# Kernel optimization log

Hardware: AMD Instinct MI355X
Metric: run time of the kernel (lower is better)

## Reference

```python
import jax, jax.numpy as jnp
import numpy as np

N_CHAINS, L, N, D, K, H, FF = 8192, 128, 100000, 256, 8, 4, 1024
LN_EPS = 1e-5  # torch LayerNorm default
EPS = 1e-8     # module eps for mean-pool denom


def _ln(x, g, b):
    mu = jnp.mean(x, axis=-1, keepdims=True)
    var = jnp.mean((x - mu) ** 2, axis=-1, keepdims=True)
    return (x - mu) * jax.lax.rsqrt(var + LN_EPS) * g + b


def setup_inputs() -> dict:
    key = jax.random.key(0)
    ks = jax.random.split(key, 24)
    s = 1.0 / np.sqrt(D)
    inp = {
        "v": jax.random.normal(ks[0], (N, D), jnp.float32),
        "batch_idx": jax.random.randint(ks[1], (N_CHAINS, L), 0, N),
        "mask": jax.random.uniform(ks[2], (N_CHAINS, L)) > 0.5,
        "count": jax.random.randint(ks[3], (N_CHAINS,), 0, 128).astype(jnp.float32),
        "rank_scores": jax.random.normal(ks[4], (N_CHAINS, L), jnp.float32),
        "pos_embed": jnp.zeros((1, K, D), jnp.float32),
        "w_qkv": jax.random.normal(ks[5], (3 * D, D), jnp.float32) * s,
        "b_qkv": jnp.zeros((3 * D,), jnp.float32),
        "w_o": jax.random.normal(ks[6], (D, D), jnp.float32) * s,
        "b_o": jnp.zeros((D,), jnp.float32),
        "ln1_g": jnp.ones((D,), jnp.float32),
        "ln1_b": jnp.zeros((D,), jnp.float32),
        "ln2_g": jnp.ones((D,), jnp.float32),
        "ln2_b": jnp.zeros((D,), jnp.float32),
        "w_ff1": jax.random.normal(ks[7], (FF, D), jnp.float32) * s,
        "b_ff1": jnp.zeros((FF,), jnp.float32),
        "w_ff2": jax.random.normal(ks[8], (D, FF), jnp.float32) / np.sqrt(FF),
        "b_ff2": jnp.zeros((D,), jnp.float32),
        "w_out1": jax.random.normal(ks[9], (FF, D + 1), jnp.float32) * s,
        "b_out1": jnp.zeros((FF,), jnp.float32),
        "w_out2": jax.random.normal(ks[10], (D, FF), jnp.float32) / np.sqrt(FF),
        "b_out2": jnp.zeros((D,), jnp.float32),
    }
    return inp


def reference(v, batch_idx, mask, count, rank_scores, pos_embed, w_qkv, b_qkv,
              w_o, b_o, ln1_g, ln1_b, ln2_g, ln2_b, w_ff1, b_ff1, w_ff2, b_ff2,
              w_out1, b_out1, w_out2, b_out2):
    neg = jnp.finfo(jnp.float32).min
    # --- top-k relevance selection among masked positions ---
    masked_scores = jnp.where(mask, rank_scores.astype(jnp.float32), neg)
    _, top_idx = jax.lax.top_k(masked_scores, K)                # [n, K]
    picked = jnp.take_along_axis(mask, top_idx, axis=1)
    sortable = jnp.where(picked, top_idx, L)                     # sentinel L
    sortable = jnp.sort(sortable, axis=1)
    picked = sortable < L
    safe_idx = jnp.where(picked, sortable, 0)                    # [n, K]
    # gather-pack: v[batch_idx][safe_idx] == v[batch_idx gathered at safe_idx]
    member_idx = jnp.take_along_axis(batch_idx, safe_idx, axis=1)
    packed = v[member_idx] * picked[..., None].astype(v.dtype)   # [n, K, D]

    x = packed + pos_embed[:, :K, :]
    kpm = ~picked                                                # True = pad
    empty = jnp.all(kpm, axis=1)
    kpm = kpm.at[:, 0].set(jnp.where(empty, False, kpm[:, 0]))

    # --- one pre-LN transformer encoder layer (gelu, dropout=0) ---
    dh = D // H
    h = _ln(x, ln1_g, ln1_b)
    qkv = h @ w_qkv.T + b_qkv                                    # [n, K, 3D]
    q, k, val = jnp.split(qkv, 3, axis=-1)
    q = q.reshape(-1, K, H, dh)
    k = k.reshape(-1, K, H, dh)
    val = val.reshape(-1, K, H, dh)
    scores = jnp.einsum('bqhd,bkhd->bhqk', q, k) / np.sqrt(dh)
    scores = jnp.where(kpm[:, None, None, :], neg, scores)
    attn = jax.nn.softmax(scores, axis=-1)
    o = jnp.einsum('bhqk,bkhd->bqhd', attn, val).reshape(-1, K, D)
    x = x + (o @ w_o.T + b_o)
    h = _ln(x, ln2_g, ln2_b)
    x = x + jax.nn.gelu(h @ w_ff1.T + b_ff1, approximate=False) @ w_ff2.T + b_ff2

    # --- masked mean pool + log-count feature + MLP head ---
    pf = picked.astype(x.dtype)
    denom = jnp.clip(jnp.sum(pf, axis=1, keepdims=True), EPS, None)
    pooled = jnp.sum(x * pf[..., None], axis=1) / denom
    pooled = jnp.where(jnp.any(picked, axis=1, keepdims=True), pooled, 0.0)
    feat = jnp.concatenate([pooled, jnp.log1p(count.astype(x.dtype))[:, None]], axis=-1)
    return jax.nn.gelu(feat @ w_out1.T + b_out1, approximate=False) @ w_out2.T + b_out2
```

## Files before the change

kernel.cpp:

```cpp
#include <hip/hip_runtime.h>


#define DIM   256
#define LSEQ  128
#define KTOK  8

typedef __bf16 bf16x8 __attribute__((ext_vector_type(8)));
typedef float  f32x4  __attribute__((ext_vector_type(4)));
typedef unsigned short u16x8 __attribute__((ext_vector_type(8)));

__device__ __forceinline__ f32x4 mfma16(bf16x8 a, bf16x8 b, f32x4 c) {
  return __builtin_amdgcn_mfma_f32_16x16x32_bf16(a, b, c, 0, 0, 0);
}

__device__ __forceinline__ unsigned short f2bf(float f) {
  unsigned u = __float_as_uint(f);
  u = (u + 0x7FFFu + ((u >> 16) & 1u)) >> 16;
  return (unsigned short)u;
}

__device__ __forceinline__ float gelu_fast(float x) {
  const float y = 0.7978845608f * __builtin_fmaf(0.044715f * x * x, x, x);
  const float e = __expf(2.f * y);
  const float t = 1.f - 2.f * __builtin_amdgcn_rcpf(e + 1.f);
  return 0.5f * x * (1.f + t);
}

struct Stage32 { u16x8 r[4]; };
__device__ __forceinline__ void stage_load(Stage32& st, const unsigned short* __restrict__ g, int tid) {
  #pragma unroll
  for (int i = 0; i < 4; ++i) st.r[i] = *(const u16x8*)&g[(tid + i * 512) * 8];
}
__device__ __forceinline__ void stage_commit(const Stage32& st, unsigned short* l, int tid) {
  #pragma unroll
  for (int i = 0; i < 4; ++i) *(u16x8*)&l[(tid + i * 512) * 8] = st.r[i];
}

__device__ __forceinline__ void pack_region(
    const float* __restrict__ src, unsigned short* __restrict__ dst,
    int g, int KC, int Ksrc, int Klim)
{
  const int ln = g & 63;
  const int t = g >> 6;
  const int s = t % KC;
  const int ntile = t / KC;
  const int row = ntile * 16 + (ln & 15);
  const int c0 = s * 32 + (ln >> 4) * 8;
  u16x8 o;
  #pragma unroll
  for (int j = 0; j < 8; ++j) {
    float val = (c0 + j < Klim) ? src[(long)row * Ksrc + c0 + j] : 0.f;
    o[j] = f2bf(val);
  }
  *(u16x8*)&dst[(long)g * 8] = o;
}

__device__ __forceinline__ void pack_region_kmaj(
    const float* __restrict__ src, unsigned short* __restrict__ dst,
    int g, int NT, int Ksrc)
{
  const int ln = g & 63;
  const int t = g >> 6;
  const int ntile = t % NT;
  const int s = t / NT;
  const int row = ntile * 16 + (ln & 15);
  const int c0 = s * 32 + (ln >> 4) * 8;
  u16x8 o;
  #pragma unroll
  for (int j = 0; j < 8; ++j) o[j] = f2bf(src[(long)row * Ksrc + c0 + j]);
  *(u16x8*)&dst[(long)g * 8] = o;
}

#define PREP_GROUPS 172032
__global__ __launch_bounds__(256) void k_prep(
    const float* __restrict__ wqkv, const float* __restrict__ wo,
    const float* __restrict__ wff1, const float* __restrict__ wff2,
    const float* __restrict__ wout1, const float* __restrict__ wout2,
    unsigned short* __restrict__ oq, unsigned short* __restrict__ oo,
    unsigned short* __restrict__ of1, unsigned short* __restrict__ of2,
    unsigned short* __restrict__ oo1, unsigned short* __restrict__ oo2)
{
  int g = blockIdx.x * 256 + threadIdx.x;
  if (g < 24576) { pack_region(wqkv, oq, g, 8, 256, 256); return; }
  g -= 24576;
  if (g < 8192)  { pack_region(wo, oo, g, 8, 256, 256); return; }
  g -= 8192;
  if (g < 32768) { pack_region(wff1, of1, g, 8, 256, 256); return; }
  g -= 32768;
  if (g < 32768) { pack_region_kmaj(wff2, of2, g, 16, 1024); return; }
  g -= 32768;
  if (g < 40960) { pack_region(wout1, oo1, g, 10, 257, 257); return; }
  g -= 40960;
  if (g < 32768) { pack_region_kmaj(wout2, oo2, g, 16, 1024); }
}

__global__ __launch_bounds__(256) void k_sel(
    const float* __restrict__ v, const int* __restrict__ batch_idx,
    const int* __restrict__ mask, const float* __restrict__ rank_scores,
    const float* __restrict__ pos_embed,
    const float* __restrict__ ln1g, const float* __restrict__ ln1b,
    float* __restrict__ X, unsigned short* __restrict__ H1p,
    int* __restrict__ NPICK)
{
  const int c = blockIdx.x;
  const int tid = threadIdx.x;
  __shared__ int s_mem[KTOK];
  __shared__ int s_np;

  if (tid < 64) {
    const int l = tid;
    unsigned long long key[2];
    #pragma unroll
    for (int t = 0; t < 2; ++t) {
      int p = l + 64 * t;
      int mk = mask[c * LSEQ + p];
      float s = rank_scores[c * LSEQ + p];
      unsigned u = __float_as_uint(s);
      u = (u & 0x80000000u) ? ~u : (u | 0x80000000u);
      unsigned long long kk =
          ((unsigned long long)u << 32) | (unsigned long long)(0xFFFFFFFFu - (unsigned)p);
      key[t] = mk ? kk : 0ull;
    }
    int w[KTOK];
    #pragma unroll
    for (int r = 0; r < KTOK; ++r) w[r] = 0x7FFFFFFF;
    int np = 0;
    for (int r = 0; r < KTOK; ++r) {
      unsigned long long best = key[0] > key[1] ? key[0] : key[1];
      for (int off = 32; off > 0; off >>= 1) {
        unsigned long long o = __shfl_xor(best, off, 64);
        if (o > best) best = o;
      }
      if (best == 0ull) break;
      int idx = (int)(0xFFFFFFFFu - (unsigned)(best & 0xFFFFFFFFull));
      w[np++] = idx;
      if (key[0] == best) key[0] = 0ull;
      if (key[1] == best) key[1] = 0ull;
    }
    #pragma unroll
    for (int a = 0; a < KTOK - 1; ++a)
      #pragma unroll
      for (int b2 = 0; b2 < KTOK - 1 - a; ++b2) {
        int x0 = w[b2], x1 = w[b2 + 1];
        w[b2] = min(x0, x1); w[b2 + 1] = max(x0, x1);
      }
    if (l < KTOK) s_mem[l] = (l < np) ? batch_idx[c * LSEQ + w[l]] : -1;
    if (l == 0) { s_np = np; NPICK[c] = np; }
  }
  __syncthreads();

  const int np = s_np;
  const int j = tid >> 5, q = tid & 31;
  const int r = s_mem[j];
  const float4* v4  = (const float4*)v;
  const float4* pe4 = (const float4*)pos_embed;
  float4* X4 = (float4*)X;

  float4 xv[2];
  #pragma unroll
  for (int rep = 0; rep < 2; ++rep) {
    const int f = 2 * q + rep;
    float4 pe = pe4[j * 64 + f];
    float4 val = make_float4(0.f, 0.f, 0.f, 0.f);
    if (j < np) val = v4[(long)r * 64 + f];
    xv[rep].x = val.x + pe.x; xv[rep].y = val.y + pe.y;
    xv[rep].z = val.z + pe.z; xv[rep].w = val.w + pe.w;
    X4[((long)c * KTOK + j) * 64 + f] = xv[rep];
  }
  float sum = 0.f, ss = 0.f;
  #pragma unroll
  for (int rep = 0; rep < 2; ++rep) {
    sum += xv[rep].x + xv[rep].y + xv[rep].z + xv[rep].w;
    ss  += xv[rep].x * xv[rep].x + xv[rep].y * xv[rep].y
         + xv[rep].z * xv[rep].z + xv[rep].w * xv[rep].w;
  }
  #pragma unroll
  for (int off = 1; off <= 16; off <<= 1) {
    sum += __shfl_xor(sum, off); ss += __shfl_xor(ss, off);
  }
  const float mu = sum * (1.f / 256.f);
  const float var = ss * (1.f / 256.f) - mu * mu;
  const float rstd = rsqrtf(var + 1e-5f);
  const int t = c * KTOK + j;
  const int mtile = t >> 4, lr = t & 15;
  const int s = q >> 2, lq = q & 3;
  u16x8 o;
  const int col = q * 8;
  o[0] = f2bf((xv[0].x - mu) * rstd * ln1g[col + 0] + ln1b[col + 0]);
  o[1] = f2bf((xv[0].y - mu) * rstd * ln1g[col + 1] + ln1b[col + 1]);
  o[2] = f2bf((xv[0].z - mu) * rstd * ln1g[col + 2] + ln1b[col + 2]);
  o[3] = f2bf((xv[0].w - mu) * rstd * ln1g[col + 3] + ln1b[col + 3]);
  o[4] = f2bf((xv[1].x - mu) * rstd * ln1g[col + 4] + ln1b[col + 4]);
  o[5] = f2bf((xv[1].y - mu) * rstd * ln1g[col + 5] + ln1b[col + 5]);
  o[6] = f2bf((xv[1].z - mu) * rstd * ln1g[col + 6] + ln1b[col + 6]);
  o[7] = f2bf((xv[1].w - mu) * rstd * ln1g[col + 7] + ln1b[col + 7]);
  *(u16x8*)&H1p[((long)(mtile * 8 + s) * 64 + lq * 16 + lr) * 8] = o;
}

__global__ __launch_bounds__(512, 4) void k_qkv(
    const unsigned short* __restrict__ H1p, unsigned short* __restrict__ QKVp,
    const unsigned short* __restrict__ wqp, const float* __restrict__ bqkv)
{
  __shared__ unsigned short buf[16384];
  __shared__ unsigned short sT[8 * 16 * 72];
  const int tid = threadIdx.x;
  const int wv = tid >> 6, ln = tid & 63;
  const int lr = ln & 15, lq = ln >> 4;
  const int mtile = blockIdx.x * 8 + wv;
  const f32x4 vzero = {0.f, 0.f, 0.f, 0.f};
  unsigned short* sTw = &sT[wv * 1152];

  bf16x8 af[8];
  #pragma unroll
  for (int s = 0; s < 8; ++s)
    af[s] = *(const bf16x8*)&H1p[((long)(mtile * 8 + s) * 64 + ln) * 8];

  Stage32 st;
  stage_load(st, wqp, tid);
  for (int c = 0; c < 12; ++c) {
    stage_commit(st, buf, tid);
    __syncthreads();
    if (c < 11) stage_load(st, wqp + (c + 1) * 16384, tid);
    f32x4 acc[4];
    #pragma unroll
    for (int nt = 0; nt < 4; ++nt) acc[nt] = vzero;
    #pragma unroll
    for (int s = 0; s < 8; ++s) {
      #pragma unroll
      for (int nt = 0; nt < 4; ++nt) {
        bf16x8 b = *(const bf16x8*)&buf[(nt * 8 + s) * 512 + ln * 8];
        acc[nt] = mfma16(af[s], b, acc[nt]);
      }
    }
    #pragma unroll
    for (int nt = 0; nt < 4; ++nt) {
      const float bias = bqkv[c * 64 + nt * 16 + lr];
      #pragma unroll
      for (int reg = 0; reg < 4; ++reg)
        sTw[(lq * 4 + reg) * 72 + nt * 16 + lr] = f2bf(acc[nt][reg] + bias);
    }
    const int r8 = ln >> 3, cg = ln & 7;
    #pragma unroll
    for (int h = 0; h < 2; ++h) {
      const int tok = h * 8 + r8;
      u16x8 vv = *(const u16x8*)&sTw[tok * 72 + cg * 8];
      *(u16x8*)&QKVp[((long)(mtile * 16 + tok)) * 768 + c * 64 + cg * 8] = vv;
    }
    __syncthreads();
  }
}

#define SQV 776

__global__ __launch_bounds__(256, 3) void k_attn(
    const unsigned short* __restrict__ QKVp, const int* __restrict__ NPICK,
    unsigned short* __restrict__ Op)
{
  __shared__ unsigned short sQKV[32 * SQV];
  __shared__ int s_np[4];
  const int tid = threadIdx.x;
  const int blk = blockIdx.x;
  if (tid < 4) s_np[tid] = NPICK[blk * 4 + tid];
  for (int i = tid; i < 3072; i += 256) {
    const int r = i / 96, u = i - r * 96;
    *(u16x8*)&sQKV[r * SQV + u * 8] =
        *(const u16x8*)&QKVp[((long)blk * 32 + r) * 768 + u * 8];
  }
  __syncthreads();
  if (tid >= 128) return;

  const int c = tid >> 5, hh = (tid >> 3) & 3, qi = tid & 7;
  const int natt = max(1, s_np[c]);
  const int qrow = c * 8 + qi;
  float sc[8];
  #pragma unroll
  for (int j = 0; j < 8; ++j) sc[j] = -1e30f;
  for (int j = 0; j < natt; ++j) {
    float d = 0.f;
    #pragma unroll
    for (int dc = 0; dc < 8; ++dc) {
      bf16x8 qv = *(const bf16x8*)&sQKV[qrow * SQV + hh * 64 + dc * 8];
      bf16x8 kv = *(const bf16x8*)&sQKV[(c * 8 + j) * SQV + 256 + hh * 64 + dc * 8];
      #pragma unroll
      for (int e = 0; e < 8; ++e) d += (float)qv[e] * (float)kv[e];
    }
    sc[j] = d * 0.125f;
  }
  float mx = -1e30f;
  #pragma unroll
  for (int j = 0; j < 8; ++j) mx = fmaxf(mx, sc[j]);
  float pr[8]; float ssum = 0.f;
  #pragma unroll
  for (int j = 0; j < 8; ++j) {
    float e = (j < natt) ? __expf(sc[j] - mx) : 0.f;
    pr[j] = e; ssum += e;
  }
  const float inv = 1.f / ssum;
  const int t = blk * 32 + qrow;
  const int mt = t >> 4, lrt = t & 15;
  #pragma unroll
  for (int dc = 0; dc < 8; ++dc) {
    float o8[8] = {0.f,0.f,0.f,0.f,0.f,0.f,0.f,0.f};
    for (int j = 0; j < natt; ++j) {
      const float pj = pr[j] * inv;
      bf16x8 vv = *(const bf16x8*)&sQKV[(c * 8 + j) * SQV + 512 + hh * 64 + dc * 8];
      #pragma unroll
      for (int e = 0; e < 8; ++e) o8[e] += pj * (float)vv[e];
    }
    u16x8 o;
    #pragma unroll
    for (int e = 0; e < 8; ++e) o[e] = f2bf(o8[e]);
    const int s = hh * 2 + (dc >> 2), lqt = dc & 3;
    *(u16x8*)&Op[((long)(mt * 8 + s) * 64 + lqt * 16 + lrt) * 8] = o;
  }
}

__global__ __launch_bounds__(512, 4) void k_oproj(
    const unsigned short* __restrict__ Op, float* __restrict__ X,
    const unsigned short* __restrict__ wop, const float* __restrict__ bo)
{
  __shared__ unsigned short buf[16384];
  __shared__ float sTf[8 * 16 * 68];
  const int tid = threadIdx.x;
  const int wv = tid >> 6, ln = tid & 63;
  const int lr = ln & 15, lq = ln >> 4;
  const int mtile = blockIdx.x * 8 + wv;
  const f32x4 vzero = {0.f, 0.f, 0.f, 0.f};
  float* sTw = &sTf[wv * 1088];

  bf16x8 af[8];
  #pragma unroll
  for (int s = 0; s < 8; ++s)
    af[s] = *(const bf16x8*)&Op[((long)(mtile * 8 + s) * 64 + ln) * 8];

  Stage32 st;
  stage_load(st, wop, tid);
  for (int c = 0; c < 4; ++c) {
    stage_commit(st, buf, tid);
    __syncthreads();
    if (c < 3) stage_load(st, wop + (c + 1) * 16384, tid);
    f32x4 acc[4];
    #pragma unroll
    for (int nt = 0; nt < 4; ++nt) acc[nt] = vzero;
    #pragma unroll
    for (int s = 0; s < 8; ++s) {
      #pragma unroll
      for (int nt = 0; nt < 4; ++nt) {
        bf16x8 b = *(const bf16x8*)&buf[(nt * 8 + s) * 512 + ln * 8];
        acc[nt] = mfma16(af[s], b, acc[nt]);
      }
    }
    #pragma unroll
    for (int nt = 0; nt < 4; ++nt) {
      const float bias = bo[c * 64 + nt * 16 + lr];
      #pragma unroll
      for (int reg = 0; reg < 4; ++reg)
        sTw[(lq * 4 + reg) * 68 + nt * 16 + lr] = acc[nt][reg] + bias;
    }
    const int r4 = ln >> 2, g4 = ln & 3;
    #pragma unroll
    for (int it = 0; it < 4; ++it) {
      const int gi = it * 4 + g4;
      f32x4 vv = *(const f32x4*)&sTw[r4 * 68 + gi * 4];
      float4* xp = (float4*)&X[((long)(mtile * 16 + r4)) * DIM + c * 64 + gi * 4];
      float4 old = *xp;
      old.x += vv[0]; old.y += vv[1]; old.z += vv[2]; old.w += vv[3];
      *xp = old;
    }
    __syncthreads();
  }
}

__global__ __launch_bounds__(256) void k_ln2(
    const float* __restrict__ X, const float* __restrict__ g,
    const float* __restrict__ b, unsigned short* __restrict__ H2p)
{
  const int tid = threadIdx.x;
  const int row = blockIdx.x * 64 + (tid >> 2);
  const int p = tid & 3;
  const float4* xr = (const float4*)(X + (long)row * DIM + p * 64);
  float4 xv[16];
  float sum = 0.f, ss = 0.f;
  #pragma unroll
  for (int i = 0; i < 16; ++i) {
    xv[i] = xr[i];
    sum += xv[i].x + xv[i].y + xv[i].z + xv[i].w;
    ss  += xv[i].x * xv[i].x + xv[i].y * xv[i].y + xv[i].z * xv[i].z + xv[i].w * xv[i].w;
  }
  sum += __shfl_xor(sum, 1); ss += __shfl_xor(ss, 1);
  sum += __shfl_xor(sum, 2); ss += __shfl_xor(ss, 2);
  const float mu = sum * (1.f / 256.f);
  const float var = ss * (1.f / 256.f) - mu * mu;
  const float rstd = rsqrtf(var + 1e-5f);
  const int mtile = row >> 4, lr = row & 15;
  #pragma unroll
  for (int i = 0; i < 16; i += 2) {
    const int q = p * 8 + (i >> 1);
    const int s = q >> 2, lq = q & 3;
    const int col = q * 8;
    u16x8 o;
    o[0] = f2bf((xv[i].x - mu) * rstd * g[col + 0] + b[col + 0]);
    o[1] = f2bf((xv[i].y - mu) * rstd * g[col + 1] + b[col + 1]);
    o[2] = f2bf((xv[i].z - mu) * rstd * g[col + 2] + b[col + 2]);
    o[3] = f2bf((xv[i].w - mu) * rstd * g[col + 3] + b[col + 3]);
    o[4] = f2bf((xv[i+1].x - mu) * rstd * g[col + 4] + b[col + 4]);
    o[5] = f2bf((xv[i+1].y - mu) * rstd * g[col + 5] + b[col + 5]);
    o[6] = f2bf((xv[i+1].z - mu) * rstd * g[col + 6] + b[col + 6]);
    o[7] = f2bf((xv[i+1].w - mu) * rstd * g[col + 7] + b[col + 7]);
    *(u16x8*)&H2p[((long)(mtile * 8 + s) * 64 + lq * 16 + lr) * 8] = o;
  }
}

#define SGPAD 72

__global__ __launch_bounds__(512, 2) void k_ff(
    float* __restrict__ X, const unsigned short* __restrict__ H2p,
    const unsigned short* __restrict__ w1p, const unsigned short* __restrict__ w2p,
    const float* __restrict__ bff1, const float* __restrict__ bff2)
{
  __shared__ unsigned short bufA[16384];
  __shared__ unsigned short bufB[16384];
  __shared__ unsigned short sG[128 * SGPAD];
  const int tid = threadIdx.x;
  const int wv = tid >> 6, ln = tid & 63;
  const int lr = ln & 15, lq = ln >> 4;
  const int m0 = wv * 16;
  const int mtile = blockIdx.x * 8 + wv;
  const f32x4 vzero = {0.f, 0.f, 0.f, 0.f};

  bf16x8 af[8];
  #pragma unroll
  for (int s = 0; s < 8; ++s)
    af[s] = *(const bf16x8*)&H2p[((long)(mtile * 8 + s) * 64 + ln) * 8];

  f32x4 acc3[16];
  #pragma unroll
  for (int nt = 0; nt < 16; ++nt) acc3[nt] = vzero;

  Stage32 stA, stB;
  stage_load(stA, w1p, tid);
  stage_load(stB, w2p, tid);

  for (int f = 0; f < 16; ++f) {
    stage_commit(stA, bufA, tid);
    stage_commit(stB, bufB, tid);
    __syncthreads();
    if (f < 15) {
      stage_load(stA, w1p + (f + 1) * 16384, tid);
      stage_load(stB, w2p + (f + 1) * 16384, tid);
    }
    f32x4 ga[4];
    #pragma unroll
    for (int nt = 0; nt < 4; ++nt) ga[nt] = vzero;
    #pragma unroll
    for (int s = 0; s < 8; ++s) {
      #pragma unroll
      for (int nt = 0; nt < 4; ++nt) {
        bf16x8 b = *(const bf16x8*)&bufA[(nt * 8 + s) * 512 + ln * 8];
        ga[nt] = mfma16(af[s], b, ga[nt]);
      }
    }
    #pragma unroll
    for (int nt = 0; nt < 4; ++nt) {
      const int n = f * 64 + nt * 16 + lr;
      const float bias = bff1[n];
      #pragma unroll
      for (int reg = 0; reg < 4; ++reg) {
        sG[(m0 + lq * 4 + reg) * SGPAD + nt * 16 + lr] = f2bf(gelu_fast(ga[nt][reg] + bias));
      }
    }
    #pragma unroll
    for (int s2 = 0; s2 < 2; ++s2) {
      bf16x8 ag = *(const bf16x8*)&sG[(m0 + lr) * SGPAD + s2 * 32 + lq * 8];
      #pragma unroll
      for (int nt = 0; nt < 16; ++nt) {
        bf16x8 b = *(const bf16x8*)&bufB[(s2 * 16 + nt) * 512 + ln * 8];
        acc3[nt] = mfma16(ag, b, acc3[nt]);
      }
    }
    __syncthreads();
  }
  #pragma unroll
  for (int nt = 0; nt < 16; ++nt) {
    const int col = nt * 16 + lr;
    const float bias = bff2[col];
    #pragma unroll
    for (int reg = 0; reg < 4; ++reg) {
      const int row = mtile * 16 + lq * 4 + reg;
      const long gi = (long)row * DIM + col;
      X[gi] = X[gi] + acc3[nt][reg] + bias;
    }
  }
}

__global__ __launch_bounds__(256) void k_pool(
    const float* __restrict__ X, const int* __restrict__ NPICK,
    const float* __restrict__ count, unsigned short* __restrict__ Fp)
{
  const int tid = threadIdx.x;
  const int cc = tid >> 3, p = tid & 7;
  const int chain = blockIdx.x * 32 + cc;
  const int np = NPICK[chain];
  const float inv = (np > 0) ? (1.f / (float)np) : 0.f;
  const int rtile = chain >> 4, lr = chain & 15;
  const float4* xb = (const float4*)(X + (long)chain * KTOK * DIM);
  #pragma unroll
  for (int i = 0; i < 8; i += 2) {
    float4 s0 = make_float4(0.f, 0.f, 0.f, 0.f);
    float4 s1 = make_float4(0.f, 0.f, 0.f, 0.f);
    for (int j = 0; j < np; ++j) {
      float4 t0 = xb[j * 64 + p * 8 + i];
      float4 t1 = xb[j * 64 + p * 8 + i + 1];
      s0.x += t0.x; s0.y += t0.y; s0.z += t0.z; s0.w += t0.w;
      s1.x += t1.x; s1.y += t1.y; s1.z += t1.z; s1.w += t1.w;
    }
    const int q = p * 4 + (i >> 1);
    const int s = q >> 2, lq = q & 3;
    u16x8 o;
    o[0] = f2bf(s0.x * inv); o[1] = f2bf(s0.y * inv);
    o[2] = f2bf(s0.z * inv); o[3] = f2bf(s0.w * inv);
    o[4] = f2bf(s1.x * inv); o[5] = f2bf(s1.y * inv);
    o[6] = f2bf(s1.z * inv); o[7] = f2bf(s1.w * inv);
    *(u16x8*)&Fp[((long)(rtile * 10 + s) * 64 + lq * 16 + lr) * 8] = o;
  }
  if (p == 7) {
    #pragma unroll
    for (int q = 32; q < 40; ++q) {
      const int s = q >> 2, lq = q & 3;
      u16x8 o = {0,0,0,0,0,0,0,0};
      if (q == 32) o[0] = f2bf(log1pf(count[chain]));
      *(u16x8*)&Fp[((long)(rtile * 10 + s) * 64 + lq * 16 + lr) * 8] = o;
    }
  }
}

__global__ __launch_bounds__(512, 2) void k_headmlp(
    const unsigned short* __restrict__ Fp,
    const unsigned short* __restrict__ wo1p, const unsigned short* __restrict__ wo2p,
    const float* __restrict__ bout1, const float* __restrict__ bout2,
    float* __restrict__ out)
{
  __shared__ unsigned short bufA[20480];
  __shared__ unsigned short bufB[16384];
  __shared__ unsigned short sG[128 * SGPAD];
  const int tid = threadIdx.x;
  const int fq = blockIdx.x & 3;
  const int mchunk = blockIdx.x >> 2;
  const int wv = tid >> 6, ln = tid & 63;
  const int lr = ln & 15, lq = ln >> 4;
  const int m0 = wv * 16;
  const int rtile = mchunk * 8 + wv;
  const f32x4 vzero = {0.f, 0.f, 0.f, 0.f};

  bf16x8 af[10];
  #pragma unroll
  for (int s = 0; s < 10; ++s)
    af[s] = *(const bf16x8*)&Fp[((long)(rtile * 10 + s) * 64 + ln) * 8];

  f32x4 oacc[16];
  #pragma unroll
  for (int nt = 0; nt < 16; ++nt) oacc[nt] = vzero;

  u16x8 rA[5]; u16x8 rB[4];
  {
    const unsigned short* a0 = wo1p + (fq * 4) * 20480;
    const unsigned short* b0 = wo2p + (fq * 4) * 16384;
    #pragma unroll
    for (int i = 0; i < 5; ++i) rA[i] = *(const u16x8*)&a0[(tid + i * 512) * 8];
    #pragma unroll
    for (int i = 0; i < 4; ++i) rB[i] = *(const u16x8*)&b0[(tid + i * 512) * 8];
  }

  for (int it = 0; it < 4; ++it) {
    const int f = fq * 4 + it;
    #pragma unroll
    for (int i = 0; i < 5; ++i) *(u16x8*)&bufA[(tid + i * 512) * 8] = rA[i];
    #pragma unroll
    for (int i = 0; i < 4; ++i) *(u16x8*)&bufB[(tid + i * 512) * 8] = rB[i];
    __syncthreads();
    if (it < 3) {
      const unsigned short* a0 = wo1p + (f + 1) * 20480;
      const unsigned short* b0 = wo2p + (f + 1) * 16384;
      #pragma unroll
      for (int i = 0; i < 5; ++i) rA[i] = *(const u16x8*)&a0[(tid + i * 512) * 8];
      #pragma unroll
      for (int i = 0; i < 4; ++i) rB[i] = *(const u16x8*)&b0[(tid + i * 512) * 8];
    }
    f32x4 ga[4];
    #pragma unroll
    for (int nt = 0; nt < 4; ++nt) ga[nt] = vzero;
    #pragma unroll
    for (int s = 0; s < 10; ++s) {
      #pragma unroll
      for (int nt = 0; nt < 4; ++nt) {
        bf16x8 b = *(const bf16x8*)&bufA[(nt * 10 + s) * 512 + ln * 8];
        ga[nt] = mfma16(af[s], b, ga[nt]);
      }
    }
    #pragma unroll
    for (int nt = 0; nt < 4; ++nt) {
      const int n = f * 64 + nt * 16 + lr;
      const float bias = bout1[n];
      #pragma unroll
      for (int reg = 0; reg < 4; ++reg) {
        sG[(m0 + lq * 4 + reg) * SGPAD + nt * 16 + lr] = f2bf(gelu_fast(ga[nt][reg] + bias));
      }
    }
    #pragma unroll
    for (int s2 = 0; s2 < 2; ++s2) {
      bf16x8 ag = *(const bf16x8*)&sG[(m0 + lr) * SGPAD + s2 * 32 + lq * 8];
      #pragma unroll
      for (int nt = 0; nt < 16; ++nt) {
        bf16x8 b = *(const bf16x8*)&bufB[(s2 * 16 + nt) * 512 + ln * 8];
        oacc[nt] = mfma16(ag, b, oacc[nt]);
      }
    }
    __syncthreads();
  }
  #pragma unroll
  for (int nt = 0; nt < 16; ++nt) {
    const int col = nt * 16 + lr;
    const float bias = (fq == 0) ? bout2[col] : 0.f;
    #pragma unroll
    for (int reg = 0; reg < 4; ++reg) {
      const int row = mchunk * 128 + m0 + lq * 4 + reg;
      atomicAdd(&out[(long)row * DIM + col], oacc[nt][reg] + bias);
    }
  }
}

extern "C" void kernel_launch(void* const* d_in, const int* in_sizes, int n_in,
                              void* d_out, int out_size, void* d_ws, size_t ws_size,
                              hipStream_t stream) {
  (void)in_sizes; (void)n_in; (void)out_size; (void)ws_size;
  const float* v          = (const float*)d_in[0];
  const int*   batch_idx  = (const int*)  d_in[1];
  const int*   mask       = (const int*)  d_in[2];
  const float* count      = (const float*)d_in[3];
  const float* rank       = (const float*)d_in[4];
  const float* pe         = (const float*)d_in[5];
  const float* w_qkv      = (const float*)d_in[6];
  const float* b_qkv      = (const float*)d_in[7];
  const float* w_o        = (const float*)d_in[8];
  const float* b_o        = (const float*)d_in[9];
  const float* ln1g       = (const float*)d_in[10];
  const float* ln1b       = (const float*)d_in[11];
  const float* ln2g       = (const float*)d_in[12];
  const float* ln2b       = (const float*)d_in[13];
  const float* w_ff1      = (const float*)d_in[14];
  const float* b_ff1      = (const float*)d_in[15];
  const float* w_ff2      = (const float*)d_in[16];
  const float* b_ff2      = (const float*)d_in[17];
  const float* w_out1     = (const float*)d_in[18];
  const float* b_out1     = (const float*)d_in[19];
  const float* w_out2     = (const float*)d_in[20];
  const float* b_out2     = (const float*)d_in[21];
  float* out = (float*)d_out;

  char* ws = (char*)d_ws;
  float*          X     = (float*)ws;
  unsigned short* H1p   = (unsigned short*)(ws + 67108864);
  unsigned short* Op    = H1p;
  unsigned short* QKVp  = (unsigned short*)(ws + 100663296);
  unsigned short* H2p   = QKVp;
  unsigned short* Fp    = (unsigned short*)(ws + 134217728);
  int*            NPICK = (int*)(ws + 201326592);
  unsigned short* wq_bf   = (unsigned short*)(ws + 201359360);
  unsigned short* wo_bf   = (unsigned short*)(ws + 201752576);
  unsigned short* wff1_bf = (unsigned short*)(ws + 201883648);
  unsigned short* wff2_bf = (unsigned short*)(ws + 202407936);
  unsigned short* wo1_bf  = (unsigned short*)(ws + 202932224);
  unsigned short* wo2_bf  = (unsigned short*)(ws + 203587584);

  k_prep<<<PREP_GROUPS / 256, 256, 0, stream>>>(
      w_qkv, w_o, w_ff1, w_ff2, w_out1, w_out2,
      wq_bf, wo_bf, wff1_bf, wff2_bf, wo1_bf, wo2_bf);

  k_sel<<<8192, 256, 0, stream>>>(v, batch_idx, mask, rank, pe,
                                  ln1g, ln1b, X, H1p, NPICK);

  k_qkv<<<512, 512, 0, stream>>>(H1p, QKVp, wq_bf, b_qkv);

  k_attn<<<2048, 256, 0, stream>>>(QKVp, NPICK, Op);

  k_oproj<<<512, 512, 0, stream>>>(Op, X, wo_bf, b_o);

  k_ln2<<<1024, 256, 0, stream>>>(X, ln2g, ln2b, H2p);

  k_ff<<<512, 512, 0, stream>>>(X, H2p, wff1_bf, wff2_bf, b_ff1, b_ff2);

  k_pool<<<256, 256, 0, stream>>>(X, NPICK, count, Fp);

  hipMemsetAsync(out, 0, (size_t)8192 * 256 * sizeof(float), stream);

  k_headmlp<<<256, 512, 0, stream>>>(Fp, wo1_bf, wo2_bf, b_out1, b_out2, out);
}
```

Measured before the change: 589.4 us.

## Fuse LN2 into o-proj, pass GELU fragments by shuffle instead of LDS

Folds the second LayerNorm into the o-projection epilogue, accumulating row sum and sum-of-squares while updating X, which removes one kernel launch and a full pass over X. In the FF and head-MLP kernels the first GEMM is computed transposed so the GELU output can be repacked into the second GEMM's A-fragment with wave shuffles. This drops the sG LDS staging buffer and lets launch bounds rise to 4 blocks per CU. The head MLP also stops prefetching weights through registers and loads them straight into LDS each iteration, which cuts register pressure but removes load/compute overlap there.

Result: slower. 737.9 us (+25.2%).

```diff
diff --git a/kernel.cpp b/kernel.cpp
--- a/kernel.cpp
+++ b/kernel.cpp
@@ -17,6 +17,10 @@
   unsigned u = __float_as_uint(f);
   u = (u + 0x7FFFu + ((u >> 16) & 1u)) >> 16;
   return (unsigned short)u;
+}
+
+__device__ __forceinline__ unsigned pack2bf(float a, float b) {
+  return (unsigned)f2bf(a) | ((unsigned)f2bf(b) << 16);
 }
 
 __device__ __forceinline__ float gelu_fast(float x) {
@@ -25,6 +29,8 @@
   const float t = 1.f - 2.f * __builtin_amdgcn_rcpf(e + 1.f);
   return 0.5f * x * (1.f + t);
 }
+
+union U4 { unsigned u[4]; bf16x8 v; };
 
 struct Stage32 { u16x8 r[4]; };
 __device__ __forceinline__ void stage_load(Stage32& st, const unsigned short* __restrict__ g, int tid) {
@@ -317,7 +323,9 @@
 
 __global__ __launch_bounds__(512, 4) void k_oproj(
     const unsigned short* __restrict__ Op, float* __restrict__ X,
-    const unsigned short* __restrict__ wop, const float* __restrict__ bo)
+    const unsigned short* __restrict__ wop, const float* __restrict__ bo,
+    const float* __restrict__ ln2g, const float* __restrict__ ln2b,
+    unsigned short* __restrict__ H2p)
 {
   __shared__ unsigned short buf[16384];
   __shared__ float sTf[8 * 16 * 68];
@@ -333,6 +341,9 @@
   for (int s = 0; s < 8; ++s)
     af[s] = *(const bf16x8*)&Op[((long)(mtile * 8 + s) * 64 + ln) * 8];
 
+  const int r4 = ln >> 2, g4 = ln & 3;
+  float lsum = 0.f, lss = 0.f;
+
   Stage32 st;
   stage_load(st, wop, tid);
   for (int c = 0; c < 4; ++c) {
@@ -357,7 +368,6 @@
       for (int reg = 0; reg < 4; ++reg)
         sTw[(lq * 4 + reg) * 68 + nt * 16 + lr] = acc[nt][reg] + bias;
     }
-    const int r4 = ln >> 2, g4 = ln & 3;
     #pragma unroll
     for (int it = 0; it < 4; ++it) {
       const int gi = it * 4 + g4;
@@ -366,65 +376,48 @@
       float4 old = *xp;
       old.x += vv[0]; old.y += vv[1]; old.z += vv[2]; old.w += vv[3];
       *xp = old;
+      lsum += old.x + old.y + old.z + old.w;
+      lss  += old.x * old.x + old.y * old.y + old.z * old.z + old.w * old.w;
     }
     __syncthreads();
   }
-}
-
-__global__ __launch_bounds__(256) void k_ln2(
-    const float* __restrict__ X, const float* __restrict__ g,
-    const float* __restrict__ b, unsigned short* __restrict__ H2p)
-{
-  const int tid = threadIdx.x;
-  const int row = blockIdx.x * 64 + (tid >> 2);
-  const int p = tid & 3;
-  const float4* xr = (const float4*)(X + (long)row * DIM + p * 64);
-  float4 xv[16];
-  float sum = 0.f, ss = 0.f;
-  #pragma unroll
-  for (int i = 0; i < 16; ++i) {
-    xv[i] = xr[i];
-    sum += xv[i].x + xv[i].y + xv[i].z + xv[i].w;
-    ss  += xv[i].x * xv[i].x + xv[i].y * xv[i].y + xv[i].z * xv[i].z + xv[i].w * xv[i].w;
-  }
-  sum += __shfl_xor(sum, 1); ss += __shfl_xor(ss, 1);
-  sum += __shfl_xor(sum, 2); ss += __shfl_xor(ss, 2);
-  const float mu = sum * (1.f / 256.f);
-  const float var = ss * (1.f / 256.f) - mu * mu;
-  const float rstd = rsqrtf(var + 1e-5f);
-  const int mtile = row >> 4, lr = row & 15;
-  #pragma unroll
-  for (int i = 0; i < 16; i += 2) {
-    const int q = p * 8 + (i >> 1);
-    const int s = q >> 2, lq = q & 3;
-    const int col = q * 8;
+  lsum += __shfl_xor(lsum, 1); lss += __shfl_xor(lss, 1);
+  lsum += __shfl_xor(lsum, 2); lss += __shfl_xor(lss, 2);
+  const float mu = lsum * (1.f / 256.f);
+  const float rstd = rsqrtf(lss * (1.f / 256.f) - mu * mu + 1e-5f);
+  const int row = mtile * 16 + r4;
+  #pragma unroll
+  for (int i = 0; i < 8; ++i) {
+    const int q = i * 4 + g4;
+    const float4 x0 = *(const float4*)&X[(long)row * DIM + q * 8];
+    const float4 x1 = *(const float4*)&X[(long)row * DIM + q * 8 + 4];
+    const float4 g0 = *(const float4*)&ln2g[q * 8];
+    const float4 g1 = *(const float4*)&ln2g[q * 8 + 4];
+    const float4 b0 = *(const float4*)&ln2b[q * 8];
+    const float4 b1 = *(const float4*)&ln2b[q * 8 + 4];
     u16x8 o;
-    o[0] = f2bf((xv[i].x - mu) * rstd * g[col + 0] + b[col + 0]);
-    o[1] = f2bf((xv[i].y - mu) * rstd * g[col + 1] + b[col + 1]);
-    o[2] = f2bf((xv[i].z - mu) * rstd * g[col + 2] + b[col + 2]);
-    o[3] = f2bf((xv[i].w - mu) * rstd * g[col + 3] + b[col + 3]);
-    o[4] = f2bf((xv[i+1].x - mu) * rstd * g[col + 4] + b[col + 4]);
-    o[5] = f2bf((xv[i+1].y - mu) * rstd * g[col + 5] + b[col + 5]);
-    o[6] = f2bf((xv[i+1].z - mu) * rstd * g[col + 6] + b[col + 6]);
-    o[7] = f2bf((xv[i+1].w - mu) * rstd * g[col + 7] + b[col + 7]);
-    *(u16x8*)&H2p[((long)(mtile * 8 + s) * 64 + lq * 16 + lr) * 8] = o;
-  }
-}
-
-#define SGPAD 72
-
-__global__ __launch_bounds__(512, 2) void k_ff(
+    o[0] = f2bf((x0.x - mu) * rstd * g0.x + b0.x);
+    o[1] = f2bf((x0.y - mu) * rstd * g0.y + b0.y);
+    o[2] = f2bf((x0.z - mu) * rstd * g0.z + b0.z);
+    o[3] = f2bf((x0.w - mu) * rstd * g0.w + b0.w);
+    o[4] = f2bf((x1.x - mu) * rstd * g1.x + b1.x);
+    o[5] = f2bf((x1.y - mu) * rstd * g1.y + b1.y);
+    o[6] = f2bf((x1.z - mu) * rstd * g1.z + b1.z);
+    o[7] = f2bf((x1.w - mu) * rstd * g1.w + b1.w);
+    *(u16x8*)&H2p[((long)(mtile * 8 + (q >> 2)) * 64 + (q & 3) * 16 + r4) * 8] = o;
+  }
+}
+
+__global__ __launch_bounds__(512, 4) void k_ff(
     float* __restrict__ X, const unsigned short* __restrict__ H2p,
     const unsigned short* __restrict__ w1p, const unsigned short* __restrict__ w2p,
     const float* __restrict__ bff1, const float* __restrict__ bff2)
 {
   __shared__ unsigned short bufA[16384];
   __shared__ unsigned short bufB[16384];
-  __shared__ unsigned short sG[128 * SGPAD];
   const int tid = threadIdx.x;
   const int wv = tid >> 6, ln = tid & 63;
   const int lr = ln & 15, lq = ln >> 4;
-  const int m0 = wv * 16;
   const int mtile = blockIdx.x * 8 + wv;
   const f32x4 vzero = {0.f, 0.f, 0.f, 0.f};
 
@@ -436,6 +429,10 @@
   f32x4 acc3[16];
   #pragma unroll
   for (int nt = 0; nt < 16; ++nt) acc3[nt] = vzero;
+
+  const int laneA = ((lq & 1) * 2) * 16 + lr;
+  const int laneB = laneA + 16;
+  const bool hi = (lq & 2) != 0;
 
   Stage32 stA, stB;
   stage_load(stA, w1p, tid);
@@ -456,26 +453,39 @@
     for (int s = 0; s < 8; ++s) {
       #pragma unroll
       for (int nt = 0; nt < 4; ++nt) {
-        bf16x8 b = *(const bf16x8*)&bufA[(nt * 8 + s) * 512 + ln * 8];
-        ga[nt] = mfma16(af[s], b, ga[nt]);
+        bf16x8 w1f = *(const bf16x8*)&bufA[(nt * 8 + s) * 512 + ln * 8];
+        ga[nt] = mfma16(w1f, af[s], ga[nt]);
       }
     }
+    unsigned p0[4], p1[4];
     #pragma unroll
     for (int nt = 0; nt < 4; ++nt) {
-      const int n = f * 64 + nt * 16 + lr;
-      const float bias = bff1[n];
-      #pragma unroll
-      for (int reg = 0; reg < 4; ++reg) {
-        sG[(m0 + lq * 4 + reg) * SGPAD + nt * 16 + lr] = f2bf(gelu_fast(ga[nt][reg] + bias));
-      }
+      const float4 b4 = *(const float4*)&bff1[f * 64 + nt * 16 + lq * 4];
+      const float g0 = gelu_fast(ga[nt][0] + b4.x);
+      const float g1 = gelu_fast(ga[nt][1] + b4.y);
+      const float g2 = gelu_fast(ga[nt][2] + b4.z);
+      const float g3 = gelu_fast(ga[nt][3] + b4.w);
+      p0[nt] = pack2bf(g0, g1);
+      p1[nt] = pack2bf(g2, g3);
     }
     #pragma unroll
     for (int s2 = 0; s2 < 2; ++s2) {
-      bf16x8 ag = *(const bf16x8*)&sG[(m0 + lr) * SGPAD + s2 * 32 + lq * 8];
+      const unsigned a0 = (unsigned)__shfl((int)p0[2 * s2],     laneA, 64);
+      const unsigned a1 = (unsigned)__shfl((int)p1[2 * s2],     laneA, 64);
+      const unsigned a2 = (unsigned)__shfl((int)p0[2 * s2],     laneB, 64);
+      const unsigned a3 = (unsigned)__shfl((int)p1[2 * s2],     laneB, 64);
+      const unsigned c0 = (unsigned)__shfl((int)p0[2 * s2 + 1], laneA, 64);
+      const unsigned c1 = (unsigned)__shfl((int)p1[2 * s2 + 1], laneA, 64);
+      const unsigned c2 = (unsigned)__shfl((int)p0[2 * s2 + 1], laneB, 64);
+      const unsigned c3 = (unsigned)__shfl((int)p1[2 * s2 + 1], laneB, 64);
+      U4 uu;
+      uu.u[0] = hi ? c0 : a0; uu.u[1] = hi ? c1 : a1;
+      uu.u[2] = hi ? c2 : a2; uu.u[3] = hi ? c3 : a3;
+      const bf16x8 gfrag = uu.v;
       #pragma unroll
       for (int nt = 0; nt < 16; ++nt) {
-        bf16x8 b = *(const bf16x8*)&bufB[(s2 * 16 + nt) * 512 + ln * 8];
-        acc3[nt] = mfma16(ag, b, acc3[nt]);
+        bf16x8 w2f = *(const bf16x8*)&bufB[(s2 * 16 + nt) * 512 + ln * 8];
+        acc3[nt] = mfma16(gfrag, w2f, acc3[nt]);
       }
     }
     __syncthreads();
@@ -534,7 +544,7 @@
   }
 }
 
-__global__ __launch_bounds__(512, 2) void k_headmlp(
+__global__ __launch_bounds__(512, 4) void k_headmlp(
     const unsigned short* __restrict__ Fp,
     const unsigned short* __restrict__ wo1p, const unsigned short* __restrict__ wo2p,
     const float* __restrict__ bout1, const float* __restrict__ bout2,
@@ -542,80 +552,78 @@
 {
   __shared__ unsigned short bufA[20480];
   __shared__ unsigned short bufB[16384];
-  __shared__ unsigned short sG[128 * SGPAD];
   const int tid = threadIdx.x;
   const int fq = blockIdx.x & 3;
   const int mchunk = blockIdx.x >> 2;
   const int wv = tid >> 6, ln = tid & 63;
   const int lr = ln & 15, lq = ln >> 4;
-  const int m0 = wv * 16;
   const int rtile = mchunk * 8 + wv;
   const f32x4 vzero = {0.f, 0.f, 0.f, 0.f};
 
-  bf16x8 af[10];
-  #pragma unroll
-  for (int s = 0; s < 10; ++s)
-    af[s] = *(const bf16x8*)&Fp[((long)(rtile * 10 + s) * 64 + ln) * 8];
-
   f32x4 oacc[16];
   #pragma unroll
   for (int nt = 0; nt < 16; ++nt) oacc[nt] = vzero;
 
-  u16x8 rA[5]; u16x8 rB[4];
-  {
-    const unsigned short* a0 = wo1p + (fq * 4) * 20480;
-    const unsigned short* b0 = wo2p + (fq * 4) * 16384;
-    #pragma unroll
-    for (int i = 0; i < 5; ++i) rA[i] = *(const u16x8*)&a0[(tid + i * 512) * 8];
-    #pragma unroll
-    for (int i = 0; i < 4; ++i) rB[i] = *(const u16x8*)&b0[(tid + i * 512) * 8];
-  }
+  const int laneA = ((lq & 1) * 2) * 16 + lr;
+  const int laneB = laneA + 16;
+  const bool hi = (lq & 2) != 0;
 
   for (int it = 0; it < 4; ++it) {
     const int f = fq * 4 + it;
-    #pragma unroll
-    for (int i = 0; i < 5; ++i) *(u16x8*)&bufA[(tid + i * 512) * 8] = rA[i];
-    #pragma unroll
-    for (int i = 0; i < 4; ++i) *(u16x8*)&bufB[(tid + i * 512) * 8] = rB[i];
     __syncthreads();
-    if (it < 3) {
-      const unsigned short* a0 = wo1p + (f + 1) * 20480;
-      const unsigned short* b0 = wo2p + (f + 1) * 16384;
-      #pragma unroll
-      for (int i = 0; i < 5; ++i) rA[i] = *(const u16x8*)&a0[(tid + i * 512) * 8];
-      #pragma unroll
-      for (int i = 0; i < 4; ++i) rB[i] = *(const u16x8*)&b0[(tid + i * 512) * 8];
-    }
+    #pragma unroll
+    for (int i = 0; i < 5; ++i)
+      *(u16x8*)&bufA[(tid + i * 512) * 8] =
+          *(const u16x8*)&wo1p[(long)f * 20480 + (tid + i * 512) * 8];
+    #pragma unroll
+    for (int i = 0; i < 4; ++i)
+      *(u16x8*)&bufB[(tid + i * 512) * 8] =
+          *(const u16x8*)&wo2p[(long)f * 16384 + (tid + i * 512) * 8];
+    __syncthreads();
+
     f32x4 ga[4];
     #pragma unroll
     for (int nt = 0; nt < 4; ++nt) ga[nt] = vzero;
     #pragma unroll
     for (int s = 0; s < 10; ++s) {
+      const bf16x8 afs = *(const bf16x8*)&Fp[((long)(rtile * 10 + s) * 64 + ln) * 8];
       #pragma unroll
       for (int nt = 0; nt < 4; ++nt) {
-        bf16x8 b = *(const bf16x8*)&bufA[(nt * 10 + s) * 512 + ln * 8];
-        ga[nt] = mfma16(af[s], b, ga[nt]);
+        bf16x8 w1f = *(const bf16x8*)&bufA[(nt * 10 + s) * 512 + ln * 8];
+        ga[nt] = mfma16(w1f, afs, ga[nt]);
       }
     }
+    unsigned p0[4], p1[4];
     #pragma unroll
     for (int nt = 0; nt < 4; ++nt) {
-      const int n = f * 64 + nt * 16 + lr;
-      const float bias = bout1[n];
-      #pragma unroll
-      for (int reg = 0; reg < 4; ++reg) {
-        sG[(m0 + lq * 4 + reg) * SGPAD + nt * 16 + lr] = f2bf(gelu_fast(ga[nt][reg] + bias));
+      const float4 b4 = *(const float4*)&bout1[f * 64 + nt * 16 + lq * 4];
+      const float g0 = gelu_fast(ga[nt][0] + b4.x);
+      const float g1 = gelu_fast(ga[nt][1] + b4.y);
+      const float g2 = gelu_fast(ga[nt][2] + b4.z);
+      const float g3 = gelu_fast(ga[nt][3] + b4.w);
+      p0[nt] = pack2bf(g0, g1);
+      p1[nt] = pack2bf(g2, g3);
+    }
+    #pragma unroll
+    for (int s2 = 0; s2 < 2; ++s2) {
+      const unsigned a0 = (unsigned)__shfl((int)p0[2 * s2],     laneA, 64);
+      const unsigned a1 = (unsigned)__shfl((int)p1[2 * s2],     laneA, 64);
+      const unsigned a2 = (unsigned)__shfl((int)p0[2 * s2],     laneB, 64);
+      const unsigned a3 = (unsigned)__shfl((int)p1[2 * s2],     laneB, 64);
+      const unsigned c0 = (unsigned)__shfl((int)p0[2 * s2 + 1], laneA, 64);
+      const unsigned c1 = (unsigned)__shfl((int)p1[2 * s2 + 1], laneA, 64);
+      const unsigned c2 = (unsigned)__shfl((int)p0[2 * s2 + 1], laneB, 64);
+      const unsigned c3 = (unsigned)__shfl((int)p1[2 * s2 + 1], laneB, 64);
+      U4 uu;
+      uu.u[0] = hi ? c0 : a0; uu.u[1] = hi ? c1 : a1;
+      uu.u[2] = hi ? c2 : a2; uu.u[3] = hi ? c3 : a3;
+      const bf16x8 gfrag = uu.v;
+      #pragma unroll
+      for (int nt = 0; nt < 16; ++nt) {
+        bf16x8 w2f = *(const bf16x8*)&bufB[(s2 * 16 + nt) * 512 + ln * 8];
+        oacc[nt] = mfma16(gfrag, w2f, oacc[nt]);
       }
     }
-    #pragma unroll
-    for (int s2 = 0; s2 < 2; ++s2) {
-      bf16x8 ag = *(const bf16x8*)&sG[(m0 + lr) * SGPAD + s2 * 32 + lq * 8];
-      #pragma unroll
-      for (int nt = 0; nt < 16; ++nt) {
-        bf16x8 b = *(const bf16x8*)&bufB[(s2 * 16 + nt) * 512 + ln * 8];
-        oacc[nt] = mfma16(ag, b, oacc[nt]);
-      }
-    }
-    __syncthreads();
   }
   #pragma unroll
   for (int nt = 0; nt < 16; ++nt) {
@@ -623,7 +631,7 @@
     const float bias = (fq == 0) ? bout2[col] : 0.f;
     #pragma unroll
     for (int reg = 0; reg < 4; ++reg) {
-      const int row = mchunk * 128 + m0 + lq * 4 + reg;
+      const int row = mchunk * 128 + wv * 16 + lq * 4 + reg;
       atomicAdd(&out[(long)row * DIM + col], oacc[nt][reg] + bias);
     }
   }
@@ -683,9 +691,7 @@
 
   k_attn<<<2048, 256, 0, stream>>>(QKVp, NPICK, Op);
 
-  k_oproj<<<512, 512, 0, stream>>>(Op, X, wo_bf, b_o);
-
-  k_ln2<<<1024, 256, 0, stream>>>(X, ln2g, ln2b, H2p);
+  k_oproj<<<512, 512, 0, stream>>>(Op, X, wo_bf, b_o, ln2g, ln2b, H2p);
 
   k_ff<<<512, 512, 0, stream>>>(X, H2p, wff1_bf, wff2_bf, b_ff1, b_ff2);
 
```
